# Performance work log

Measured on AMD Instinct MI355X. Metric: run time of the kernel, lower is better.

The kernel has to match this reference:

```python
import jax, jax.numpy as jnp
import numpy as np

N = 131072      # number of nodes / samples
IN_DIM = 128    # input_dim
H = 128         # hidden_dim
OUT_DIM = 10    # output_dim


def setup_inputs() -> dict:
    key = jax.random.key(0)
    ks = jax.random.split(key, 20)
    s = 0.05
    def rn(k, shape):
        return jax.random.normal(k, shape, jnp.float32) * s
    return {
        "x": jax.random.normal(ks[0], (N, IN_DIM), jnp.float32),
        # GRU layer 1 (seq_len=1, h0=0 => weight_hh contributes nothing; only b_hh matters)
        "w_ih_f1": rn(ks[1], (3 * H, IN_DIM)), "b_ih_f1": rn(ks[2], (3 * H,)), "b_hh_f1": rn(ks[3], (3 * H,)),
        "w_ih_b1": rn(ks[4], (3 * H, IN_DIM)), "b_ih_b1": rn(ks[5], (3 * H,)), "b_hh_b1": rn(ks[6], (3 * H,)),
        # GRU layer 2 (input 2H)
        "w_ih_f2": rn(ks[7], (3 * H, 2 * H)), "b_ih_f2": rn(ks[8], (3 * H,)), "b_hh_f2": rn(ks[9], (3 * H,)),
        "w_ih_b2": rn(ks[10], (3 * H, 2 * H)), "b_ih_b2": rn(ks[11], (3 * H,)), "b_hh_b2": rn(ks[12], (3 * H,)),
        # GCNConv layers
        "w_g1": rn(ks[13], (2 * H, 128)), "b_g1": rn(ks[14], (128,)),
        "w_g2": rn(ks[15], (128, 64)), "b_g2": rn(ks[16], (64,)),
        # final fc
        "w_fc": rn(ks[17], (64, OUT_DIM)), "b_fc": rn(ks[18], (OUT_DIM,)),
    }


def _gru_cell_zero(x, w_ih, b_ih, b_hh):
    # PyTorch GRU cell with h_prev = 0: h' = (1 - z) * n_gate
    gi = x @ w_ih.T + b_ih                    # [n, 3H]
    ir, iz, inn = jnp.split(gi, 3, axis=-1)
    hr, hz, hn = jnp.split(b_hh, 3)
    r = jax.nn.sigmoid(ir + hr)
    z = jax.nn.sigmoid(iz + hz)
    ng = jnp.tanh(inn + r * hn)
    return (1.0 - z) * ng


def _gcn(x, w, b, sources, targets, n):
    # PyG GCNConv: D^{-1/2}(A+I)D^{-1/2} X W + b, self-loops already in edge lists
    xw = x @ w                                 # [n, out]
    deg = jax.ops.segment_sum(jnp.ones(sources.shape[0], x.dtype), targets, num_segments=n)
    dinv = jax.lax.rsqrt(deg)
    norm = dinv[sources] * dinv[targets]       # [E]
    msg = norm[:, None] * xw[sources]          # gather
    return jax.ops.segment_sum(msg, targets, num_segments=n) + b  # scatter-add


def reference(x, w_ih_f1, b_ih_f1, b_hh_f1, w_ih_b1, b_ih_b1, b_hh_b1,
              w_ih_f2, b_ih_f2, b_hh_f2, w_ih_b2, b_ih_b2, b_hh_b2,
              w_g1, b_g1, w_g2, b_g2, w_fc, b_fc):
    n = x.shape[0]
    # seq_len = 1 => bidirectional GRU output is [fwd_cell(x); bwd_cell(x)]
    h1 = jnp.concatenate([_gru_cell_zero(x, w_ih_f1, b_ih_f1, b_hh_f1),
                          _gru_cell_zero(x, w_ih_b1, b_ih_b1, b_hh_b1)], axis=-1)
    h2 = jnp.concatenate([_gru_cell_zero(h1, w_ih_f2, b_ih_f2, b_hh_f2),
                          _gru_cell_zero(h1, w_ih_b2, b_ih_b2, b_hh_b2)], axis=-1)
    # chain graph, both directions, plus self loops (GCNConv adds them)
    src = jnp.arange(n - 1)
    dst = jnp.arange(1, n)
    ar = jnp.arange(n)
    sources = jnp.concatenate([src, dst, ar])
    targets = jnp.concatenate([dst, src, ar])
    g1 = _gcn(h2, w_g1, b_g1, sources, targets, n)   # dropout is identity in eval
    g2 = _gcn(g1, w_g2, b_g2, sources, targets, n)
    return g2 @ w_fc + b_fc
```

## Files before the change

kernel.cpp:

```cpp
#include <hip/hip_runtime.h>
#include <stdint.h>

#define N_NODES 131072
#define HDIM 128

typedef __bf16 bf16x8 __attribute__((ext_vector_type(8)));
typedef float f32x4 __attribute__((ext_vector_type(4)));
typedef unsigned short us8 __attribute__((ext_vector_type(8)));
typedef unsigned short ushort_t;

__device__ __forceinline__ float bf2f(ushort_t u) {
    union { float f; uint32_t i; } v; v.i = ((uint32_t)u) << 16; return v.f;
}
__device__ __forceinline__ ushort_t f2bf(float f) {
    union { float f; uint32_t i; } v; v.f = f;
    uint32_t i = v.i;
    return (ushort_t)((i + 0x7FFFu + ((i >> 16) & 1u)) >> 16);
}

__device__ __forceinline__ void gll16(const ushort_t* g, ushort_t* l) {
    __builtin_amdgcn_global_load_lds(
        (const __attribute__((address_space(1))) uint32_t*)g,
        (__attribute__((address_space(3))) uint32_t*)l, 16, 0, 0);
}

__device__ __forceinline__ bf16x8 ldsw(const ushort_t* base, int R, int g) {
    return *(const bf16x8*)&base[R * 64 + (((g - R) & 7) << 3)];
}

__device__ __forceinline__ float fsig(float x) {
    return __builtin_amdgcn_rcpf(1.0f + __expf(-x));
}
__device__ __forceinline__ float ftanh(float y) {
    float yc = fminf(fmaxf(y, -15.0f), 15.0f);
    float e = __expf(2.0f * yc);
    return (e - 1.0f) * __builtin_amdgcn_rcpf(e + 1.0f);
}

template<int NC>
__device__ __forceinline__ void swz(int b, int& m, int& c) {
    int mhi = b / (8 * NC);
    int rem = b - mhi * (8 * NC);
    c = rem >> 3;
    m = mhi * 8 + (rem & 7);
}

__global__ __launch_bounds__(256) void prep_all(
    const float* __restrict__ w_f1, const float* __restrict__ w_b1,
    const float* __restrict__ w_f2, const float* __restrict__ w_b2,
    ushort_t* __restrict__ PWF1, ushort_t* __restrict__ PWB1,
    ushort_t* __restrict__ PWF2, ushort_t* __restrict__ PWB2,
    const float* __restrict__ w_g1, const float* __restrict__ b_g1,
    const float* __restrict__ w_g2, const float* __restrict__ b_g2,
    const float* __restrict__ w_fc, const float* __restrict__ b_fc,
    ushort_t* __restrict__ M16, float* __restrict__ cc)
{
    __shared__ float wfc_s[640];
    __shared__ float T1[128][10];
    const int t = threadIdx.x;

    if (blockIdx.x < 1152) {
        int idx = blockIdx.x * 256 + t;
        if (idx < 49152) {
            PWF1[idx] = f2bf(w_f1[idx]);
        } else if (idx < 98304) {
            int j = idx - 49152;  PWB1[j] = f2bf(w_b1[j]);
        } else if (idx < 196608) {
            int j = idx - 98304;  PWF2[j] = f2bf(w_f2[j]);
        } else if (idx < 294912) {
            int j = idx - 196608; PWB2[j] = f2bf(w_b2[j]);
        }
        return;
    }

    for (int i = t; i < 640; i += 256) wfc_s[i] = w_fc[i];
    __syncthreads();
    if (t < 128) {
        float s[10];
        #pragma unroll
        for (int j = 0; j < 10; ++j) s[j] = 0.0f;
        const float4* row = (const float4*)(w_g2 + t * 64);
        #pragma unroll
        for (int k4 = 0; k4 < 16; ++k4) {
            float4 v = row[k4];
            #pragma unroll
            for (int j = 0; j < 10; ++j)
                s[j] += v.x * wfc_s[(k4 * 4 + 0) * 10 + j] + v.y * wfc_s[(k4 * 4 + 1) * 10 + j]
                      + v.z * wfc_s[(k4 * 4 + 2) * 10 + j] + v.w * wfc_s[(k4 * 4 + 3) * 10 + j];
        }
        #pragma unroll
        for (int j = 0; j < 10; ++j) T1[t][j] = s[j];
    }
    __syncthreads();
    float m[10];
    #pragma unroll
    for (int j = 0; j < 10; ++j) m[j] = 0.0f;
    const float4* row1 = (const float4*)(w_g1 + t * 128);
    #pragma unroll 4
    for (int k4 = 0; k4 < 32; ++k4) {
        float4 v = row1[k4];
        #pragma unroll
        for (int j = 0; j < 10; ++j)
            m[j] += v.x * T1[k4 * 4 + 0][j] + v.y * T1[k4 * 4 + 1][j]
                  + v.z * T1[k4 * 4 + 2][j] + v.w * T1[k4 * 4 + 3][j];
    }
    #pragma unroll
    for (int j = 0; j < 16; ++j)
        M16[j * 256 + t] = (j < 10) ? f2bf(m[j]) : (ushort_t)0;
    if (t < 10) {
        float s1 = 0.0f;
        for (int k2 = 0; k2 < 128; ++k2) s1 += b_g1[k2] * T1[k2][t];
        cc[t] = s1;
        float s2 = 0.0f;
        for (int k3 = 0; k3 < 64; ++k3) s2 += b_g2[k3] * wfc_s[k3 * 10 + t];
        cc[16 + t] = s2 + b_fc[t];
    }
}

__global__ __launch_bounds__(256, 7) void gru_l1(
    const float* __restrict__ X,
    const ushort_t* __restrict__ Wf,
    const ushort_t* __restrict__ Wb,
    const float* __restrict__ bi_f, const float* __restrict__ bh_f,
    const float* __restrict__ bi_b, const float* __restrict__ bh_b,
    ushort_t* __restrict__ Hout)
{
    __shared__ ushort_t As[64 * 64];
    __shared__ ushort_t Bs[96 * 64];
    const int tid = threadIdx.x;
    int mt, comb;
    swz<8>(blockIdx.x, mt, comb);
    const int m0 = mt * 64;
    const int dir = comb >> 2;
    const int j0 = (comb & 3) * 32;
    const ushort_t* W = dir ? Wb : Wf;
    const float* b_ih = dir ? bi_b : bi_f;
    const float* b_hh = dir ? bh_b : bh_f;
    const int coloff = dir << 7;

    const int wv = tid >> 6, lane = tid & 63;
    const int lr = lane & 15, lq = lane >> 4;
    const int tr = tid >> 3, tc = tid & 7;
    const int sc = ((tr + tc) & 7) << 3;

    f32x4 acc[3][2];
    #pragma unroll
    for (int g = 0; g < 3; ++g)
        #pragma unroll
        for (int ct = 0; ct < 2; ++ct)
            #pragma unroll
            for (int e = 0; e < 4; ++e) acc[g][ct][e] = 0.0f;

    for (int t = 0; t < 2; ++t) {
        const int k0 = t * 64;
        const float* ga = X + (size_t)(m0 + tr) * 128 + k0 + sc;
        float4 fa[2][2];
        #pragma unroll
        for (int i = 0; i < 2; ++i) {
            const float4* p = (const float4*)(ga + (size_t)i * 32 * 128);
            fa[i][0] = p[0]; fa[i][1] = p[1];
        }
        #pragma unroll
        for (int i = 0; i < 3; ++i) {
            int wr = (i << 7) + j0 + ((i * 32 + tr) % 96 == (i * 32 + tr) ? 0 : 0);
            (void)wr;
        }
        #pragma unroll
        for (int i = 0; i < 3; ++i) {
            int br_ = i * 32 + tr;
            int g = br_ >> 5;
            int wr = (g << 7) + j0 + (br_ & 31);
            gll16(W + (size_t)wr * 128 + k0 + sc, &Bs[(i * 256 + tid) * 8]);
        }
        #pragma unroll
        for (int i = 0; i < 2; ++i) {
            bf16x8 t8;
            t8[0] = (__bf16)fa[i][0].x; t8[1] = (__bf16)fa[i][0].y;
            t8[2] = (__bf16)fa[i][0].z; t8[3] = (__bf16)fa[i][0].w;
            t8[4] = (__bf16)fa[i][1].x; t8[5] = (__bf16)fa[i][1].y;
            t8[6] = (__bf16)fa[i][1].z; t8[7] = (__bf16)fa[i][1].w;
            *(bf16x8*)&As[(i * 256 + tid) * 8] = t8;
        }
        __syncthreads();
        #pragma unroll
        for (int kk = 0; kk < 64; kk += 32) {
            const int g8 = (kk >> 3) + lq;
            bf16x8 a0 = ldsw(As, wv * 16 + lr, g8);
            #pragma unroll
            for (int g = 0; g < 3; ++g) {
                #pragma unroll
                for (int ct = 0; ct < 2; ++ct) {
                    bf16x8 b = ldsw(Bs, g * 32 + ct * 16 + lr, g8);
                    acc[g][ct] = __builtin_amdgcn_mfma_f32_16x16x32_bf16(a0, b, acc[g][ct], 0, 0, 0);
                }
            }
        }
        __syncthreads();
    }

    #pragma unroll
    for (int ct = 0; ct < 2; ++ct) {
        const int j = j0 + ct * 16 + lr;
        const float br  = b_ih[j] + b_hh[j];
        const float bz  = b_ih[HDIM + j] + b_hh[HDIM + j];
        const float bn  = b_ih[2 * HDIM + j];
        const float bhn = b_hh[2 * HDIM + j];
        #pragma unroll
        for (int r = 0; r < 4; ++r) {
            const int row = m0 + wv * 16 + lq * 4 + r;
            float rg = fsig(acc[0][ct][r] + br);
            float zg = fsig(acc[1][ct][r] + bz);
            float ng = ftanh(acc[2][ct][r] + bn + rg * bhn);
            ((__bf16*)Hout)[(size_t)row * 256 + coloff + j] = (__bf16)((1.0f - zg) * ng);
        }
    }
}

__global__ __launch_bounds__(256, 8) void gru_l2(
    const ushort_t* __restrict__ A,
    const ushort_t* __restrict__ Wf,
    const ushort_t* __restrict__ Wb,
    const float* __restrict__ bi_f, const float* __restrict__ bh_f,
    const float* __restrict__ bi_b, const float* __restrict__ bh_b,
    const ushort_t* __restrict__ M16,
    float* __restrict__ Zp)
{
    __shared__ ushort_t As[64 * 64];
    __shared__ ushort_t Bs[96 * 64];
    const int tid = threadIdx.x;
    int mt, comb;
    swz<8>(blockIdx.x, mt, comb);
    const int m0 = mt * 64;
    const int dir = comb >> 2;
    const int j0 = (comb & 3) * 32;
    const ushort_t* W = dir ? Wb : Wf;
    const float* b_ih = dir ? bi_b : bi_f;
    const float* b_hh = dir ? bh_b : bh_f;
    const int coloff = dir << 7;

    const int wv = tid >> 6, lane = tid & 63;
    const int lr = lane & 15, lq = lane >> 4;
    const int tr = tid >> 3, tc = tid & 7;
    const int sc = ((tr + tc) & 7) << 3;

    f32x4 acc[3][2];
    #pragma unroll
    for (int g = 0; g < 3; ++g)
        #pragma unroll
        for (int ct = 0; ct < 2; ++ct)
            #pragma unroll
            for (int e = 0; e < 4; ++e) acc[g][ct][e] = 0.0f;

    for (int t = 0; t < 4; ++t) {
        const int k0 = t * 64;
        const ushort_t* ga = A + (size_t)(m0 + tr) * 256 + k0 + sc;
        #pragma unroll
        for (int i = 0; i < 2; ++i)
            gll16(ga + (size_t)i * 32 * 256, &As[(i * 256 + tid) * 8]);
        #pragma unroll
        for (int i = 0; i < 3; ++i) {
            int br_ = i * 32 + tr;
            int g = br_ >> 5;
            int wr = (g << 7) + j0 + (br_ & 31);
            gll16(W + (size_t)wr * 256 + k0 + sc, &Bs[(i * 256 + tid) * 8]);
        }
        __syncthreads();
        #pragma unroll
        for (int kk = 0; kk < 64; kk += 32) {
            const int g8 = (kk >> 3) + lq;
            bf16x8 a0 = ldsw(As, wv * 16 + lr, g8);
            #pragma unroll
            for (int g = 0; g < 3; ++g) {
                #pragma unroll
                for (int ct = 0; ct < 2; ++ct) {
                    bf16x8 b = ldsw(Bs, g * 32 + ct * 16 + lr, g8);
                    acc[g][ct] = __builtin_amdgcn_mfma_f32_16x16x32_bf16(a0, b, acc[g][ct], 0, 0, 0);
                }
            }
        }
        __syncthreads();
    }

    const bf16x8 mb = *(const bf16x8*)&M16[lr * 256 + coloff + j0 + lq * 8];

    ushort_t* hs = &As[wv * 640];
    #pragma unroll
    for (int ct = 0; ct < 2; ++ct) {
        const int j = j0 + ct * 16 + lr;
        const float br  = b_ih[j] + b_hh[j];
        const float bz  = b_ih[HDIM + j] + b_hh[HDIM + j];
        const float bn  = b_ih[2 * HDIM + j];
        const float bhn = b_hh[2 * HDIM + j];
        #pragma unroll
        for (int r = 0; r < 4; ++r) {
            const int lrow = lq * 4 + r;
            float rg = fsig(acc[0][ct][r] + br);
            float zg = fsig(acc[1][ct][r] + bz);
            float ng = ftanh(acc[2][ct][r] + bn + rg * bhn);
            ((__bf16*)hs)[lrow * 40 + ct * 16 + lr] = (__bf16)((1.0f - zg) * ng);
        }
    }
    __syncthreads();

    bf16x8 ha0 = *(const bf16x8*)&hs[lr * 40 + lq * 8];
    f32x4 z0;
    #pragma unroll
    for (int e = 0; e < 4; ++e) z0[e] = 0.0f;
    z0 = __builtin_amdgcn_mfma_f32_16x16x32_bf16(ha0, mb, z0, 0, 0, 0);

    if (lr < 10) {
        float* zslice = Zp + (size_t)comb * ((size_t)N_NODES * 10);
        #pragma unroll
        for (int r = 0; r < 4; ++r)
            zslice[(size_t)(m0 + wv * 16 + lq * 4 + r) * 10 + lr] = z0[r];
    }
}

__global__ __launch_bounds__(256) void zsum(
    const float4* __restrict__ Zp4, float4* __restrict__ Zc4)
{
    int i = blockIdx.x * 256 + threadIdx.x;
    float4 a = Zp4[i];
    #pragma unroll
    for (int s = 1; s < 8; ++s) {
        float4 b = Zp4[(size_t)s * 327680 + i];
        a.x += b.x; a.y += b.y; a.z += b.z; a.w += b.w;
    }
    Zc4[i] = a;
}

__device__ __forceinline__ float dcoef(int i) {
    return (i == 0 || i == N_NODES - 1) ? 0.70710678118654752f : 0.57735026918962576f;
}
__global__ __launch_bounds__(256) void st5(
    const float* __restrict__ z, float* __restrict__ out,
    const float* __restrict__ cc)
{
    int idx = blockIdx.x * 256 + threadIdx.x;
    int i = idx >> 4, c = idx & 15;
    if (c >= 10) return;
    float d_i = dcoef(i);
    float accv = 0.0f, dsum = d_i;
    #pragma unroll
    for (int oj = -1; oj <= 1; ++oj) {
        int j = i + oj;
        if (j < 0 || j >= N_NODES) continue;
        float dj = dcoef(j);
        if (oj != 0) dsum += dj;
        float wj = 0.0f;
        #pragma unroll
        for (int ok = -1; ok <= 1; ++ok) {
            int k = j + ok;
            if (k < 0 || k >= N_NODES) continue;
            wj += dcoef(k) * z[(size_t)k * 10 + c];
        }
        accv += dj * dj * wj;
    }
    out[(size_t)i * 10 + c] = d_i * accv + d_i * dsum * cc[c] + cc[16 + c];
}

extern "C" void kernel_launch(void* const* d_in, const int* in_sizes, int n_in,
                              void* d_out, int out_size, void* d_ws, size_t ws_size,
                              hipStream_t stream) {
    const float* x     = (const float*)d_in[0];
    const float* w_f1  = (const float*)d_in[1];
    const float* bi_f1 = (const float*)d_in[2];
    const float* bh_f1 = (const float*)d_in[3];
    const float* w_b1  = (const float*)d_in[4];
    const float* bi_b1 = (const float*)d_in[5];
    const float* bh_b1 = (const float*)d_in[6];
    const float* w_f2  = (const float*)d_in[7];
    const float* bi_f2 = (const float*)d_in[8];
    const float* bh_f2 = (const float*)d_in[9];
    const float* w_b2  = (const float*)d_in[10];
    const float* bi_b2 = (const float*)d_in[11];
    const float* bh_b2 = (const float*)d_in[12];
    const float* w_g1  = (const float*)d_in[13];
    const float* b_g1  = (const float*)d_in[14];
    const float* w_g2  = (const float*)d_in[15];
    const float* b_g2  = (const float*)d_in[16];
    const float* w_fc  = (const float*)d_in[17];
    const float* b_fc  = (const float*)d_in[18];

    char* ws = (char*)d_ws;
    ushort_t* h1   = (ushort_t*)(ws);
    float*    Zp   = (float*)(ws + 67108864);
    float*    Zc   = (float*)(ws + 109051904);
    ushort_t* PWF1 = (ushort_t*)(ws + 134217728);
    ushort_t* PWB1 = PWF1 + 49152;
    ushort_t* PWF2 = PWB1 + 49152;
    ushort_t* PWB2 = PWF2 + 98304;
    ushort_t* M16  = PWB2 + 98304;
    float*    cc   = (float*)(M16 + 4096);

    prep_all<<<1153, 256, 0, stream>>>(w_f1, w_b1, w_f2, w_b2,
                                       PWF1, PWB1, PWF2, PWB2,
                                       w_g1, b_g1, w_g2, b_g2, w_fc, b_fc,
                                       M16, cc);

    gru_l1<<<N_NODES / 64 * 8, 256, 0, stream>>>(
        x, PWF1, PWB1, bi_f1, bh_f1, bi_b1, bh_b1, h1);
    gru_l2<<<N_NODES / 64 * 8, 256, 0, stream>>>(
        h1, PWF2, PWB2, bi_f2, bh_f2, bi_b2, bh_b2, M16, Zp);

    zsum<<<1280, 256, 0, stream>>>((const float4*)Zp, (float4*)Zc);
    st5<<<N_NODES * 16 / 256, 256, 0, stream>>>(Zc, (float*)d_out, cc);
}
```

Baseline: 311.5 us.

## Make GRU blocks own 128-row tiles across all column chunks, drop partial-sum pass

Each GRU block now covers 128 rows with 512 threads and loops over all eight direction/column chunks. It loads its activation tile into LDS once instead of re-reading it in eight separate blocks. Layer 2 accumulates the projected output in registers across chunks, so the 8-way partial buffer and the zsum reduction kernel are removed. The stencil kernel now stages neighbour rows in LDS. The cost is a larger LDS footprint, fewer and bigger blocks, and serialized weight reloads inside each block, which may reduce occupancy and latency hiding.

Result: faster. 270.2 us, median of 2 (-13.3%).

```diff
diff --git a/kernel.cpp b/kernel.cpp
--- a/kernel.cpp
+++ b/kernel.cpp
@@ -6,12 +6,8 @@
 
 typedef __bf16 bf16x8 __attribute__((ext_vector_type(8)));
 typedef float f32x4 __attribute__((ext_vector_type(4)));
-typedef unsigned short us8 __attribute__((ext_vector_type(8)));
 typedef unsigned short ushort_t;
 
-__device__ __forceinline__ float bf2f(ushort_t u) {
-    union { float f; uint32_t i; } v; v.i = ((uint32_t)u) << 16; return v.f;
-}
 __device__ __forceinline__ ushort_t f2bf(float f) {
     union { float f; uint32_t i; } v; v.f = f;
     uint32_t i = v.i;
@@ -35,14 +31,6 @@
     float yc = fminf(fmaxf(y, -15.0f), 15.0f);
     float e = __expf(2.0f * yc);
     return (e - 1.0f) * __builtin_amdgcn_rcpf(e + 1.0f);
-}
-
-template<int NC>
-__device__ __forceinline__ void swz(int b, int& m, int& c) {
-    int mhi = b / (8 * NC);
-    int rem = b - mhi * (8 * NC);
-    c = rem >> 3;
-    m = mhi * 8 + (rem & 7);
 }
 
 __global__ __launch_bounds__(256) void prep_all(
@@ -117,7 +105,7 @@
     }
 }
 
-__global__ __launch_bounds__(256, 7) void gru_l1(
+__global__ __launch_bounds__(512, 4) void gru_l1(
     const float* __restrict__ X,
     const ushort_t* __restrict__ Wf,
     const ushort_t* __restrict__ Wb,
@@ -125,238 +113,250 @@
     const float* __restrict__ bi_b, const float* __restrict__ bh_b,
     ushort_t* __restrict__ Hout)
 {
-    __shared__ ushort_t As[64 * 64];
+    __shared__ ushort_t As[2 * 8192];
     __shared__ ushort_t Bs[96 * 64];
     const int tid = threadIdx.x;
-    int mt, comb;
-    swz<8>(blockIdx.x, mt, comb);
-    const int m0 = mt * 64;
-    const int dir = comb >> 2;
-    const int j0 = (comb & 3) * 32;
-    const ushort_t* W = dir ? Wb : Wf;
-    const float* b_ih = dir ? bi_b : bi_f;
-    const float* b_hh = dir ? bh_b : bh_f;
-    const int coloff = dir << 7;
-
+    const int m0 = blockIdx.x * 128;
     const int wv = tid >> 6, lane = tid & 63;
     const int lr = lane & 15, lq = lane >> 4;
-    const int tr = tid >> 3, tc = tid & 7;
-    const int sc = ((tr + tc) & 7) << 3;
-
-    f32x4 acc[3][2];
-    #pragma unroll
-    for (int g = 0; g < 3; ++g)
-        #pragma unroll
-        for (int ct = 0; ct < 2; ++ct)
-            #pragma unroll
-            for (int e = 0; e < 4; ++e) acc[g][ct][e] = 0.0f;
-
-    for (int t = 0; t < 2; ++t) {
-        const int k0 = t * 64;
-        const float* ga = X + (size_t)(m0 + tr) * 128 + k0 + sc;
-        float4 fa[2][2];
-        #pragma unroll
-        for (int i = 0; i < 2; ++i) {
-            const float4* p = (const float4*)(ga + (size_t)i * 32 * 128);
-            fa[i][0] = p[0]; fa[i][1] = p[1];
-        }
-        #pragma unroll
-        for (int i = 0; i < 3; ++i) {
-            int wr = (i << 7) + j0 + ((i * 32 + tr) % 96 == (i * 32 + tr) ? 0 : 0);
-            (void)wr;
-        }
-        #pragma unroll
-        for (int i = 0; i < 3; ++i) {
-            int br_ = i * 32 + tr;
-            int g = br_ >> 5;
-            int wr = (g << 7) + j0 + (br_ & 31);
-            gll16(W + (size_t)wr * 128 + k0 + sc, &Bs[(i * 256 + tid) * 8]);
-        }
-        #pragma unroll
-        for (int i = 0; i < 2; ++i) {
-            bf16x8 t8;
-            t8[0] = (__bf16)fa[i][0].x; t8[1] = (__bf16)fa[i][0].y;
-            t8[2] = (__bf16)fa[i][0].z; t8[3] = (__bf16)fa[i][0].w;
-            t8[4] = (__bf16)fa[i][1].x; t8[5] = (__bf16)fa[i][1].y;
-            t8[6] = (__bf16)fa[i][1].z; t8[7] = (__bf16)fa[i][1].w;
-            *(bf16x8*)&As[(i * 256 + tid) * 8] = t8;
-        }
-        __syncthreads();
-        #pragma unroll
-        for (int kk = 0; kk < 64; kk += 32) {
-            const int g8 = (kk >> 3) + lq;
-            bf16x8 a0 = ldsw(As, wv * 16 + lr, g8);
-            #pragma unroll
-            for (int g = 0; g < 3; ++g) {
+
+    #pragma unroll
+    for (int p = 0; p < 4; ++p) {
+        int ci = p * 512 + tid;
+        int reg = ci >> 10, w = ci & 1023, row = w >> 3, slot = w & 7;
+        int g = (slot + row) & 7;
+        const float* src = X + (size_t)(m0 + row) * 128 + reg * 64 + g * 8;
+        float4 f0 = ((const float4*)src)[0];
+        float4 f1 = ((const float4*)src)[1];
+        bf16x8 t8;
+        t8[0] = (__bf16)f0.x; t8[1] = (__bf16)f0.y; t8[2] = (__bf16)f0.z; t8[3] = (__bf16)f0.w;
+        t8[4] = (__bf16)f1.x; t8[5] = (__bf16)f1.y; t8[6] = (__bf16)f1.z; t8[7] = (__bf16)f1.w;
+        *(bf16x8*)&As[ci * 8] = t8;
+    }
+    __syncthreads();
+
+    for (int jc = 0; jc < 8; ++jc) {
+        const int dir = jc >> 2;
+        const int j0 = (jc & 3) * 32;
+        const ushort_t* W = dir ? Wb : Wf;
+        const float* b_ih = dir ? bi_b : bi_f;
+        const float* b_hh = dir ? bh_b : bh_f;
+        const int coloff = dir << 7;
+
+        f32x4 acc[3][2];
+        #pragma unroll
+        for (int g = 0; g < 3; ++g)
+            #pragma unroll
+            for (int ct = 0; ct < 2; ++ct)
                 #pragma unroll
-                for (int ct = 0; ct < 2; ++ct) {
-                    bf16x8 b = ldsw(Bs, g * 32 + ct * 16 + lr, g8);
-                    acc[g][ct] = __builtin_amdgcn_mfma_f32_16x16x32_bf16(a0, b, acc[g][ct], 0, 0, 0);
+                for (int e = 0; e < 4; ++e) acc[g][ct][e] = 0.0f;
+
+        for (int t = 0; t < 2; ++t) {
+            {
+                int ci = tid;
+                int r96 = ci >> 3, slot = ci & 7, g = (slot + r96) & 7;
+                int wr = ((r96 >> 5) << 7) + j0 + (r96 & 31);
+                gll16(W + (size_t)wr * 128 + t * 64 + g * 8, &Bs[ci * 8]);
+                if (tid < 256) {
+                    int ci2 = 512 + tid;
+                    int r2 = ci2 >> 3, s2 = ci2 & 7, g2 = (s2 + r2) & 7;
+                    int wr2 = ((r2 >> 5) << 7) + j0 + (r2 & 31);
+                    gll16(W + (size_t)wr2 * 128 + t * 64 + g2 * 8, &Bs[ci2 * 8]);
                 }
             }
-        }
-        __syncthreads();
-    }
-
-    #pragma unroll
-    for (int ct = 0; ct < 2; ++ct) {
-        const int j = j0 + ct * 16 + lr;
-        const float br  = b_ih[j] + b_hh[j];
-        const float bz  = b_ih[HDIM + j] + b_hh[HDIM + j];
-        const float bn  = b_ih[2 * HDIM + j];
-        const float bhn = b_hh[2 * HDIM + j];
-        #pragma unroll
-        for (int r = 0; r < 4; ++r) {
-            const int row = m0 + wv * 16 + lq * 4 + r;
-            float rg = fsig(acc[0][ct][r] + br);
-            float zg = fsig(acc[1][ct][r] + bz);
-            float ng = ftanh(acc[2][ct][r] + bn + rg * bhn);
-            ((__bf16*)Hout)[(size_t)row * 256 + coloff + j] = (__bf16)((1.0f - zg) * ng);
-        }
-    }
-}
-
-__global__ __launch_bounds__(256, 8) void gru_l2(
+            __syncthreads();
+            #pragma unroll
+            for (int kk = 0; kk < 64; kk += 32) {
+                const int g8 = (kk >> 3) + lq;
+                bf16x8 a0 = ldsw(&As[t * 8192], wv * 16 + lr, g8);
+                #pragma unroll
+                for (int g = 0; g < 3; ++g) {
+                    #pragma unroll
+                    for (int ct = 0; ct < 2; ++ct) {
+                        bf16x8 b = ldsw(Bs, g * 32 + ct * 16 + lr, g8);
+                        acc[g][ct] = __builtin_amdgcn_mfma_f32_16x16x32_bf16(a0, b, acc[g][ct], 0, 0, 0);
+                    }
+                }
+            }
+            __syncthreads();
+        }
+
+        #pragma unroll
+        for (int ct = 0; ct < 2; ++ct) {
+            const int j = j0 + ct * 16 + lr;
+            const float br  = b_ih[j] + b_hh[j];
+            const float bz  = b_ih[HDIM + j] + b_hh[HDIM + j];
+            const float bn  = b_ih[2 * HDIM + j];
+            const float bhn = b_hh[2 * HDIM + j];
+            #pragma unroll
+            for (int r = 0; r < 4; ++r) {
+                const int row = m0 + wv * 16 + lq * 4 + r;
+                float rg = fsig(acc[0][ct][r] + br);
+                float zg = fsig(acc[1][ct][r] + bz);
+                float ng = ftanh(acc[2][ct][r] + bn + rg * bhn);
+                ((__bf16*)Hout)[(size_t)row * 256 + coloff + j] = (__bf16)((1.0f - zg) * ng);
+            }
+        }
+    }
+}
+
+__global__ __launch_bounds__(512, 4) void gru_l2(
     const ushort_t* __restrict__ A,
     const ushort_t* __restrict__ Wf,
     const ushort_t* __restrict__ Wb,
     const float* __restrict__ bi_f, const float* __restrict__ bh_f,
     const float* __restrict__ bi_b, const float* __restrict__ bh_b,
     const ushort_t* __restrict__ M16,
-    float* __restrict__ Zp)
+    float* __restrict__ Zc)
 {
-    __shared__ ushort_t As[64 * 64];
+    __shared__ ushort_t Ah[4 * 8192];
     __shared__ ushort_t Bs[96 * 64];
     const int tid = threadIdx.x;
-    int mt, comb;
-    swz<8>(blockIdx.x, mt, comb);
-    const int m0 = mt * 64;
-    const int dir = comb >> 2;
-    const int j0 = (comb & 3) * 32;
-    const ushort_t* W = dir ? Wb : Wf;
-    const float* b_ih = dir ? bi_b : bi_f;
-    const float* b_hh = dir ? bh_b : bh_f;
-    const int coloff = dir << 7;
-
+    const int m0 = blockIdx.x * 128;
     const int wv = tid >> 6, lane = tid & 63;
     const int lr = lane & 15, lq = lane >> 4;
-    const int tr = tid >> 3, tc = tid & 7;
-    const int sc = ((tr + tc) & 7) << 3;
-
-    f32x4 acc[3][2];
-    #pragma unroll
-    for (int g = 0; g < 3; ++g)
-        #pragma unroll
-        for (int ct = 0; ct < 2; ++ct)
-            #pragma unroll
-            for (int e = 0; e < 4; ++e) acc[g][ct][e] = 0.0f;
-
-    for (int t = 0; t < 4; ++t) {
-        const int k0 = t * 64;
-        const ushort_t* ga = A + (size_t)(m0 + tr) * 256 + k0 + sc;
-        #pragma unroll
-        for (int i = 0; i < 2; ++i)
-            gll16(ga + (size_t)i * 32 * 256, &As[(i * 256 + tid) * 8]);
-        #pragma unroll
-        for (int i = 0; i < 3; ++i) {
-            int br_ = i * 32 + tr;
-            int g = br_ >> 5;
-            int wr = (g << 7) + j0 + (br_ & 31);
-            gll16(W + (size_t)wr * 256 + k0 + sc, &Bs[(i * 256 + tid) * 8]);
-        }
+
+    #pragma unroll
+    for (int p = 0; p < 8; ++p) {
+        int ci = p * 512 + tid;
+        int reg = ci >> 10, w = ci & 1023, row = w >> 3, slot = w & 7;
+        int g = (slot + row) & 7;
+        gll16(A + (size_t)(m0 + row) * 256 + reg * 64 + g * 8, &Ah[ci * 8]);
+    }
+    __syncthreads();
+
+    f32x4 z;
+    #pragma unroll
+    for (int e = 0; e < 4; ++e) z[e] = 0.0f;
+
+    for (int jc = 0; jc < 8; ++jc) {
+        const int dir = jc >> 2;
+        const int j0 = (jc & 3) * 32;
+        const ushort_t* W = dir ? Wb : Wf;
+        const float* b_ih = dir ? bi_b : bi_f;
+        const float* b_hh = dir ? bh_b : bh_f;
+        const int coloff = dir << 7;
+
+        f32x4 acc[3][2];
+        #pragma unroll
+        for (int g = 0; g < 3; ++g)
+            #pragma unroll
+            for (int ct = 0; ct < 2; ++ct)
+                #pragma unroll
+                for (int e = 0; e < 4; ++e) acc[g][ct][e] = 0.0f;
+
+        for (int t = 0; t < 4; ++t) {
+            {
+                int ci = tid;
+                int r96 = ci >> 3, slot = ci & 7, g = (slot + r96) & 7;
+                int wr = ((r96 >> 5) << 7) + j0 + (r96 & 31);
+                gll16(W + (size_t)wr * 256 + t * 64 + g * 8, &Bs[ci * 8]);
+                if (tid < 256) {
+                    int ci2 = 512 + tid;
+                    int r2 = ci2 >> 3, s2 = ci2 & 7, g2 = (s2 + r2) & 7;
+                    int wr2 = ((r2 >> 5) << 7) + j0 + (r2 & 31);
+                    gll16(W + (size_t)wr2 * 256 + t * 64 + g2 * 8, &Bs[ci2 * 8]);
+                }
+            }
+            __syncthreads();
+            #pragma unroll
+            for (int kk = 0; kk < 64; kk += 32) {
+                const int g8 = (kk >> 3) + lq;
+                bf16x8 a0 = ldsw(&Ah[t * 8192], wv * 16 + lr, g8);
+                #pragma unroll
+                for (int g = 0; g < 3; ++g) {
+                    #pragma unroll
+                    for (int ct = 0; ct < 2; ++ct) {
+                        bf16x8 b = ldsw(Bs, g * 32 + ct * 16 + lr, g8);
+                        acc[g][ct] = __builtin_amdgcn_mfma_f32_16x16x32_bf16(a0, b, acc[g][ct], 0, 0, 0);
+                    }
+                }
+            }
+            __syncthreads();
+        }
+
+        const bf16x8 mb = *(const bf16x8*)&M16[lr * 256 + coloff + j0 + lq * 8];
+
+        ushort_t* hs = &Bs[wv * 640];
+        #pragma unroll
+        for (int ct = 0; ct < 2; ++ct) {
+            const int j = j0 + ct * 16 + lr;
+            const float br  = b_ih[j] + b_hh[j];
+            const float bz  = b_ih[HDIM + j] + b_hh[HDIM + j];
+            const float bn  = b_ih[2 * HDIM + j];
+            const float bhn = b_hh[2 * HDIM + j];
+            #pragma unroll
+            for (int r = 0; r < 4; ++r) {
+                const int lrow = lq * 4 + r;
+                float rg = fsig(acc[0][ct][r] + br);
+                float zg = fsig(acc[1][ct][r] + bz);
+                float ng = ftanh(acc[2][ct][r] + bn + rg * bhn);
+                ((__bf16*)hs)[lrow * 40 + ct * 16 + lr] = (__bf16)((1.0f - zg) * ng);
+            }
+        }
+        bf16x8 ha = *(const bf16x8*)&hs[lr * 40 + lq * 8];
+        z = __builtin_amdgcn_mfma_f32_16x16x32_bf16(ha, mb, z, 0, 0, 0);
         __syncthreads();
-        #pragma unroll
-        for (int kk = 0; kk < 64; kk += 32) {
-            const int g8 = (kk >> 3) + lq;
-            bf16x8 a0 = ldsw(As, wv * 16 + lr, g8);
-            #pragma unroll
-            for (int g = 0; g < 3; ++g) {
-                #pragma unroll
-                for (int ct = 0; ct < 2; ++ct) {
-                    bf16x8 b = ldsw(Bs, g * 32 + ct * 16 + lr, g8);
-                    acc[g][ct] = __builtin_amdgcn_mfma_f32_16x16x32_bf16(a0, b, acc[g][ct], 0, 0, 0);
-                }
-            }
-        }
-        __syncthreads();
-    }
-
-    const bf16x8 mb = *(const bf16x8*)&M16[lr * 256 + coloff + j0 + lq * 8];
-
-    ushort_t* hs = &As[wv * 640];
-    #pragma unroll
-    for (int ct = 0; ct < 2; ++ct) {
-        const int j = j0 + ct * 16 + lr;
-        const float br  = b_ih[j] + b_hh[j];
-        const float bz  = b_ih[HDIM + j] + b_hh[HDIM + j];
-        const float bn  = b_ih[2 * HDIM + j];
-        const float bhn = b_hh[2 * HDIM + j];
-        #pragma unroll
-        for (int r = 0; r < 4; ++r) {
-            const int lrow = lq * 4 + r;
-            float rg = fsig(acc[0][ct][r] + br);
-            float zg = fsig(acc[1][ct][r] + bz);
-            float ng = ftanh(acc[2][ct][r] + bn + rg * bhn);
-            ((__bf16*)hs)[lrow * 40 + ct * 16 + lr] = (__bf16)((1.0f - zg) * ng);
-        }
-    }
-    __syncthreads();
-
-    bf16x8 ha0 = *(const bf16x8*)&hs[lr * 40 + lq * 8];
-    f32x4 z0;
-    #pragma unroll
-    for (int e = 0; e < 4; ++e) z0[e] = 0.0f;
-    z0 = __builtin_amdgcn_mfma_f32_16x16x32_bf16(ha0, mb, z0, 0, 0, 0);
+    }
 
     if (lr < 10) {
-        float* zslice = Zp + (size_t)comb * ((size_t)N_NODES * 10);
         #pragma unroll
         for (int r = 0; r < 4; ++r)
-            zslice[(size_t)(m0 + wv * 16 + lq * 4 + r) * 10 + lr] = z0[r];
-    }
-}
-
-__global__ __launch_bounds__(256) void zsum(
-    const float4* __restrict__ Zp4, float4* __restrict__ Zc4)
-{
-    int i = blockIdx.x * 256 + threadIdx.x;
-    float4 a = Zp4[i];
-    #pragma unroll
-    for (int s = 1; s < 8; ++s) {
-        float4 b = Zp4[(size_t)s * 327680 + i];
-        a.x += b.x; a.y += b.y; a.z += b.z; a.w += b.w;
-    }
-    Zc4[i] = a;
+            Zc[(size_t)(m0 + wv * 16 + lq * 4 + r) * 10 + lr] = z[r];
+    }
 }
 
 __device__ __forceinline__ float dcoef(int i) {
     return (i == 0 || i == N_NODES - 1) ? 0.70710678118654752f : 0.57735026918962576f;
 }
-__global__ __launch_bounds__(256) void st5(
-    const float* __restrict__ z, float* __restrict__ out,
+__global__ __launch_bounds__(256) void stz(
+    const float* __restrict__ Zc, float* __restrict__ out,
     const float* __restrict__ cc)
 {
-    int idx = blockIdx.x * 256 + threadIdx.x;
-    int i = idx >> 4, c = idx & 15;
-    if (c >= 10) return;
-    float d_i = dcoef(i);
-    float accv = 0.0f, dsum = d_i;
-    #pragma unroll
-    for (int oj = -1; oj <= 1; ++oj) {
-        int j = i + oj;
-        if (j < 0 || j >= N_NODES) continue;
-        float dj = dcoef(j);
-        if (oj != 0) dsum += dj;
-        float wj = 0.0f;
-        #pragma unroll
-        for (int ok = -1; ok <= 1; ++ok) {
-            int k = j + ok;
-            if (k < 0 || k >= N_NODES) continue;
-            wj += dcoef(k) * z[(size_t)k * 10 + c];
-        }
-        accv += dj * dj * wj;
-    }
-    out[(size_t)i * 10 + c] = d_i * accv + d_i * dsum * cc[c] + cc[16 + c];
+    __shared__ __align__(16) float zl[2600];
+    const int tid = threadIdx.x;
+    const int n0 = blockIdx.x * 256;
+    const bool edge = (blockIdx.x == 0) || (blockIdx.x == gridDim.x - 1);
+
+    if (!edge) {
+        const size_t base4 = ((size_t)n0 * 10 - 20) >> 2;
+        const float4* Z4 = (const float4*)Zc;
+        for (int i4 = tid; i4 < 650; i4 += 256)
+            ((float4*)zl)[i4] = Z4[base4 + i4];
+    } else {
+        for (int i = tid; i < 2600; i += 256) {
+            int nl = i / 10;
+            int c = i - nl * 10;
+            int n = n0 - 2 + nl;
+            zl[i] = (n >= 0 && n < N_NODES) ? Zc[(size_t)n * 10 + c] : 0.0f;
+        }
+    }
+    __syncthreads();
+
+    const int i = n0 + tid;
+    const float d_i = dcoef(i);
+    float dsum = d_i;
+    if (i - 1 >= 0) dsum += dcoef(i - 1);
+    if (i + 1 < N_NODES) dsum += dcoef(i + 1);
+
+    #pragma unroll
+    for (int c = 0; c < 10; ++c) {
+        float accv = 0.0f;
+        #pragma unroll
+        for (int oj = -1; oj <= 1; ++oj) {
+            int j = i + oj;
+            if (j < 0 || j >= N_NODES) continue;
+            float dj = dcoef(j);
+            float wj = 0.0f;
+            #pragma unroll
+            for (int ok = -1; ok <= 1; ++ok) {
+                int k = j + ok;
+                wj += dcoef(k) * zl[(tid + 2 + oj + ok) * 10 + c];
+            }
+            accv += dj * dj * wj;
+        }
+        out[(size_t)i * 10 + c] = d_i * accv + d_i * dsum * cc[c] + cc[16 + c];
+    }
 }
 
 extern "C" void kernel_launch(void* const* d_in, const int* in_sizes, int n_in,
@@ -384,8 +384,7 @@
 
     char* ws = (char*)d_ws;
     ushort_t* h1   = (ushort_t*)(ws);
-    float*    Zp   = (float*)(ws + 67108864);
-    float*    Zc   = (float*)(ws + 109051904);
+    float*    Zc   = (float*)(ws + 67108864);
     ushort_t* PWF1 = (ushort_t*)(ws + 134217728);
     ushort_t* PWB1 = PWF1 + 49152;
     ushort_t* PWF2 = PWB1 + 49152;
@@ -398,11 +397,10 @@
                                        w_g1, b_g1, w_g2, b_g2, w_fc, b_fc,
                                        M16, cc);
 
-    gru_l1<<<N_NODES / 64 * 8, 256, 0, stream>>>(
+    gru_l1<<<N_NODES / 128, 512, 0, stream>>>(
         x, PWF1, PWB1, bi_f1, bh_f1, bi_b1, bh_b1, h1);
-    gru_l2<<<N_NODES / 64 * 8, 256, 0, stream>>>(
-        h1, PWF2, PWB2, bi_f2, bh_f2, bi_b2, bh_b2, M16, Zp);
-
-    zsum<<<1280, 256, 0, stream>>>((const float4*)Zp, (float4*)Zc);
-    st5<<<N_NODES * 16 / 256, 256, 0, stream>>>(Zc, (float*)d_out, cc);
-}
+    gru_l2<<<N_NODES / 128, 512, 0, stream>>>(
+        h1, PWF2, PWB2, bi_f2, bh_f2, bi_b2, bh_b2, M16, Zc);
+
+    stz<<<N_NODES / 256, 256, 0, stream>>>(Zc, (float*)d_out, cc);
+}
```
